# Kernel tuning notes

Hardware: AMD Instinct MI355X
Metric: run time of the kernel (lower is better)

The kernel has to match this reference:

```python
import jax, jax.numpy as jnp
import numpy as np
import math

N = 512  # num particles
D = 128  # particle dimension


def setup_inputs() -> dict:
    key = jax.random.key(0)
    particles = jax.random.normal(key, (N, D), dtype=jnp.float32)
    return {"particles": particles}


def reference(particles):
    # particles: [N, D]
    n = particles.shape[0]
    # delta_x[i, j] = particles[j] - particles[i]  (matches unsqueeze(0) - unsqueeze(1))
    delta_x = particles[None, :, :] - particles[:, None, :]   # [N, N, D]
    norm_sq = delta_x * delta_x                               # [N, N, D]

    # mode='univ': per-dimension median over strictly-upper-triangular pairs
    iu_r, iu_c = np.triu_indices(n, k=1)                      # static indices
    sel = norm_sq[iu_r, iu_c, :]                              # [M, D], M = N(N-1)/2
    m = sel.shape[0]
    # torch.median returns the LOWER of the two middle values for even counts
    median = jnp.sort(sel, axis=0)[(m - 1) // 2]              # [D]

    h = median / math.log(n + 1)
    bandwidth = jnp.maximum(h, jnp.asarray(1e-9, dtype=h.dtype))  # [D]

    log_kernel = -(norm_sq / bandwidth)                       # [N, N, D]
    grad_log_kernel = -2.0 * delta_x / bandwidth              # [N, N, D]
    return log_kernel, grad_log_kernel
```

## Files before the change

kernel.cpp:

```cpp
#include <hip/hip_runtime.h>
#include <hip/hip_bf16.h>

#define NP 512
#define DD 128

__global__ void __launch_bounds__(512)
median_bw_kernel(const float* __restrict__ particles, float* __restrict__ inv_bw)
{
    const int d   = blockIdx.x;
    const int tid = threadIdx.x;

    __shared__ float v[NP];
    __shared__ int   cnt_s[2][8];

    float r = particles[tid * DD + d];

    for (int k = 2; k <= NP; k <<= 1) {
        for (int s = k >> 1; s > 0; s >>= 1) {
            float other;
            if (s < 64) {
                other = __shfl_xor(r, s);
            } else {
                __syncthreads();
                v[tid] = r;
                __syncthreads();
                other = v[tid ^ s];
            }
            const bool lower = (tid & s) == 0;
            const bool up    = (tid & k) == 0;
            r = (lower == up) ? fminf(r, other) : fmaxf(r, other);
        }
    }
    __syncthreads();
    v[tid] = r;
    __syncthreads();

    const float vj = r;
    const int want1 = (NP * (NP - 1) / 2 - 1) / 2 + 1;

    const float maxd = v[NP - 1] - v[0];
    unsigned lo = 0u;
    unsigned hi = __float_as_uint(maxd) + 1u;

    int A = 0, B = tid;
    int buf = 0;

    while (lo < hi) {
        const unsigned mid = (lo + hi) >> 1;
        const float x = __uint_as_float(mid);

        int a = A, b = B;
        while (a < b) {
            const int m = (a + b) >> 1;
            if (vj - v[m] <= x) b = m; else a = m + 1;
        }
        int cnt = tid - a;

        #pragma unroll
        for (int off = 32; off > 0; off >>= 1)
            cnt += __shfl_down(cnt, off);
        if ((tid & 63) == 0) cnt_s[buf][tid >> 6] = cnt;
        __syncthreads();

        int tot = 0;
        #pragma unroll
        for (int w = 0; w < 8; ++w) tot += cnt_s[buf][w];

        if (tot >= want1) { hi = mid;      A = a; }
        else             { lo = mid + 1u; B = a; }
        buf ^= 1;
    }

    if (tid == 0) {
        const float Dk     = __uint_as_float(lo);
        const float median = Dk * Dk;
        const float h      = median / 6.240275844172107f;
        const float bw     = fmaxf(h, 1e-9f);
        inv_bw[d] = 1.0f / bw;
    }
}

__global__ void __launch_bounds__(256)
stein_out_kernel(const float* __restrict__ particles,
                 const float* __restrict__ inv_bw,
                 float4* __restrict__ out_lk,
                 float4* __restrict__ out_g)
{
    const float4* __restrict__ p4  = (const float4*)particles;
    const float4* __restrict__ ib4 = (const float4*)inv_bw;
    const int total = NP * NP * (DD / 4);

    for (int t = blockIdx.x * blockDim.x + threadIdx.x; t < total;
         t += gridDim.x * blockDim.x) {
        const int d4 = t & (DD / 4 - 1);
        const int j  = (t >> 5) & (NP - 1);
        const int i  = t >> 14;

        const float4 xj = p4[j * (DD / 4) + d4];
        const float4 xi = p4[i * (DD / 4) + d4];
        const float4 ib = ib4[d4];

        float4 lk, g;
        {
            const float dx = xj.x - xi.x;
            lk.x = -(dx * dx * ib.x);
            g.x  = -2.0f * dx * ib.x;
        }
        {
            const float dx = xj.y - xi.y;
            lk.y = -(dx * dx * ib.y);
            g.y  = -2.0f * dx * ib.y;
        }
        {
            const float dx = xj.z - xi.z;
            lk.z = -(dx * dx * ib.z);
            g.z  = -2.0f * dx * ib.z;
        }
        {
            const float dx = xj.w - xi.w;
            lk.w = -(dx * dx * ib.w);
            g.w  = -2.0f * dx * ib.w;
        }
        out_lk[t] = lk;
        out_g[t]  = g;
    }
}

extern "C" void kernel_launch(void* const* d_in, const int* in_sizes, int n_in,
                              void* d_out, int out_size, void* d_ws, size_t ws_size,
                              hipStream_t stream)
{
    const float* particles = (const float*)d_in[0];
    float* out    = (float*)d_out;
    float* inv_bw = (float*)d_ws;

    median_bw_kernel<<<DD, 512, 0, stream>>>(particles, inv_bw);

    float4* out_lk = (float4*)out;
    float4* out_g  = (float4*)(out + (size_t)NP * NP * DD);
    stein_out_kernel<<<2048, 256, 0, stream>>>(particles, inv_bw, out_lk, out_g);
}
```

Before: 72.27 us.

## Run median binary search in a single wavefront and use nontemporal output stores

The bandwidth median search now runs on one 64-lane wavefront, with each lane handling eight sorted elements. This removes the per-iteration __syncthreads and the shared-memory count reduction, and uses a wave-wide xor shuffle reduction instead. The output kernel writes both result arrays with nontemporal stores to reduce cache pollution on a large streaming write. The tradeoff is that the median phase now uses less parallelism, since seven of the eight waves sit idle and each lane does eight serial searches per iteration.

```diff
diff --git a/kernel.cpp b/kernel.cpp
--- a/kernel.cpp
+++ b/kernel.cpp
@@ -3,6 +3,8 @@
 
 #define NP 512
 #define DD 128
+
+typedef float f4_ext __attribute__((ext_vector_type(4)));
 
 __global__ void __launch_bounds__(512)
 median_bw_kernel(const float* __restrict__ particles, float* __restrict__ inv_bw)
@@ -11,7 +13,6 @@
     const int tid = threadIdx.x;
 
     __shared__ float v[NP];
-    __shared__ int   cnt_s[2][8];
 
     float r = particles[tid * DD + d];
 
@@ -35,48 +36,72 @@
     v[tid] = r;
     __syncthreads();
 
-    const float vj = r;
-    const int want1 = (NP * (NP - 1) / 2 - 1) / 2 + 1;
+    if (tid < 64) {
+        const int lane  = tid;
+        const int want1 = (NP * (NP - 1) / 2 - 1) / 2 + 1;
 
-    const float maxd = v[NP - 1] - v[0];
-    unsigned lo = 0u;
-    unsigned hi = __float_as_uint(maxd) + 1u;
+        float vj[8];
+        int   A[8], B[8];
+        #pragma unroll
+        for (int w = 0; w < 8; ++w) {
+            const int j = lane + 64 * w;
+            vj[w] = v[j];
+            A[w]  = 0;
+            B[w]  = j;
+        }
 
-    int A = 0, B = tid;
-    int buf = 0;
+        const float maxd = v[NP - 1] - v[0];
+        unsigned lo = 0u;
+        unsigned hi = __float_as_uint(maxd) + 1u;
 
-    while (lo < hi) {
-        const unsigned mid = (lo + hi) >> 1;
-        const float x = __uint_as_float(mid);
+        while (lo < hi) {
+            const unsigned mid = (lo + hi) >> 1;
+            const float x = __uint_as_float(mid);
 
-        int a = A, b = B;
-        while (a < b) {
-            const int m = (a + b) >> 1;
-            if (vj - v[m] <= x) b = m; else a = m + 1;
+            int a[8], b[8];
+            #pragma unroll
+            for (int w = 0; w < 8; ++w) { a[w] = A[w]; b[w] = B[w]; }
+
+            for (int step = 0; step < 10; ++step) {
+                bool any = false;
+                #pragma unroll
+                for (int w = 0; w < 8; ++w) {
+                    if (a[w] < b[w]) {
+                        const int m = (a[w] + b[w]) >> 1;
+                        const float pv = v[m];
+                        if (vj[w] - pv <= x) b[w] = m; else a[w] = m + 1;
+                        any = true;
+                    }
+                }
+                if (!any) break;
+            }
+
+            int cnt = 0;
+            #pragma unroll
+            for (int w = 0; w < 8; ++w) cnt += (lane + 64 * w) - a[w];
+
+            #pragma unroll
+            for (int off = 1; off < 64; off <<= 1)
+                cnt += __shfl_xor(cnt, off);
+
+            if (cnt >= want1) {
+                hi = mid;
+                #pragma unroll
+                for (int w = 0; w < 8; ++w) A[w] = a[w];
+            } else {
+                lo = mid + 1u;
+                #pragma unroll
+                for (int w = 0; w < 8; ++w) B[w] = a[w];
+            }
         }
-        int cnt = tid - a;
 
-        #pragma unroll
-        for (int off = 32; off > 0; off >>= 1)
-            cnt += __shfl_down(cnt, off);
-        if ((tid & 63) == 0) cnt_s[buf][tid >> 6] = cnt;
-        __syncthreads();
-
-        int tot = 0;
-        #pragma unroll
-        for (int w = 0; w < 8; ++w) tot += cnt_s[buf][w];
-
-        if (tot >= want1) { hi = mid;      A = a; }
-        else             { lo = mid + 1u; B = a; }
-        buf ^= 1;
-    }
-
-    if (tid == 0) {
-        const float Dk     = __uint_as_float(lo);
-        const float median = Dk * Dk;
-        const float h      = median / 6.240275844172107f;
-        const float bw     = fmaxf(h, 1e-9f);
-        inv_bw[d] = 1.0f / bw;
+        if (lane == 0) {
+            const float Dk     = __uint_as_float(lo);
+            const float median = Dk * Dk;
+            const float h      = median / 6.240275844172107f;
+            const float bw     = fmaxf(h, 1e-9f);
+            inv_bw[d] = 1.0f / bw;
+        }
     }
 }
 
@@ -121,8 +146,8 @@
             lk.w = -(dx * dx * ib.w);
             g.w  = -2.0f * dx * ib.w;
         }
-        out_lk[t] = lk;
-        out_g[t]  = g;
+        __builtin_nontemporal_store(*(const f4_ext*)&lk, (f4_ext*)&out_lk[t]);
+        __builtin_nontemporal_store(*(const f4_ext*)&g,  (f4_ext*)&out_g[t]);
     }
 }
 
```

Result: slower. 132.0 us (+82.7%).

## Speed median search with order-statistic bracketing, interpolation, and final candidate sort

Applied to the files above, without the earlier changes.

The bisection over float bit patterns for the pairwise-difference median is changed. It now starts from brackets taken from the min and max of fixed-lag sorted differences, alternates interpolation steps with bisection steps, and stops once at most 512 candidate pairs remain. Those candidates are compacted into shared memory with a prefix scan and sorted with a second bitonic sort to select the exact rank. This is meant to cut the number of barrier-synchronized counting rounds in the median kernel. The cost is extra reductions, a scan and a second sort, and the lag-150 bracket heuristic relies on the input distribution for its benefit.

```diff
diff --git a/kernel.cpp b/kernel.cpp
--- a/kernel.cpp
+++ b/kernel.cpp
@@ -4,17 +4,8 @@
 #define NP 512
 #define DD 128
 
-__global__ void __launch_bounds__(512)
-median_bw_kernel(const float* __restrict__ particles, float* __restrict__ inv_bw)
-{
-    const int d   = blockIdx.x;
-    const int tid = threadIdx.x;
-
-    __shared__ float v[NP];
-    __shared__ int   cnt_s[2][8];
-
-    float r = particles[tid * DD + d];
-
+__device__ __forceinline__ float bitonic512(float r, int tid, float* lds)
+{
     for (int k = 2; k <= NP; k <<= 1) {
         for (int s = k >> 1; s > 0; s >>= 1) {
             float other;
@@ -22,15 +13,34 @@
                 other = __shfl_xor(r, s);
             } else {
                 __syncthreads();
-                v[tid] = r;
+                lds[tid] = r;
                 __syncthreads();
-                other = v[tid ^ s];
+                other = lds[tid ^ s];
             }
             const bool lower = (tid & s) == 0;
             const bool up    = (tid & k) == 0;
             r = (lower == up) ? fminf(r, other) : fmaxf(r, other);
         }
     }
+    return r;
+}
+
+__global__ void __launch_bounds__(512)
+median_bw_kernel(const float* __restrict__ particles, float* __restrict__ inv_bw)
+{
+    const int d    = blockIdx.x;
+    const int tid  = threadIdx.x;
+    const int lane = tid & 63;
+    const int wid  = tid >> 6;
+
+    __shared__ float v[NP];
+    __shared__ float cand[NP];
+    __shared__ int   cnt_s[2][8];
+    __shared__ float red_s[2][8];
+    __shared__ int   scan_s[8];
+
+    float r = particles[tid * DD + d];
+    r = bitonic512(r, tid, v);
     __syncthreads();
     v[tid] = r;
     __syncthreads();
@@ -38,45 +48,107 @@
     const float vj = r;
     const int want1 = (NP * (NP - 1) / 2 - 1) / 2 + 1;
 
+    const float d150 = (tid >= 150) ? (vj - v[tid - 150]) : 0.0f;
+    float dmn = (tid >= 150) ? d150 : INFINITY;
+    float dmx = d150;
+    #pragma unroll
+    for (int off = 32; off > 0; off >>= 1) {
+        dmn = fminf(dmn, __shfl_xor(dmn, off));
+        dmx = fmaxf(dmx, __shfl_xor(dmx, off));
+    }
+    if (lane == 0) { red_s[0][wid] = dmn; red_s[1][wid] = dmx; }
+    __syncthreads();
+    float g_mn = INFINITY, g_mx = 0.0f;
+    #pragma unroll
+    for (int w = 0; w < 8; ++w) {
+        g_mn = fminf(g_mn, red_s[0][w]);
+        g_mx = fmaxf(g_mx, red_s[1][w]);
+    }
+
     const float maxd = v[NP - 1] - v[0];
     unsigned lo = 0u;
     unsigned hi = __float_as_uint(maxd) + 1u;
-
+    int C_lo = 0;
+    int C_hi = NP * (NP - 1) / 2;
     int A = 0, B = tid;
-    int buf = 0;
+    int buf = 0, round = 0;
+    int T = C_hi - C_lo;
 
     while (lo < hi) {
-        const unsigned mid = (lo + hi) >> 1;
+        T = C_hi - C_lo;
+        if (T <= NP) break;
+
+        unsigned mid;
+        if (round == 0)      mid = __float_as_uint(g_mn);
+        else if (round == 1) mid = __float_as_uint(g_mx);
+        else if (round & 1) {
+            const float flo  = __uint_as_float(lo);
+            const float fhi  = __uint_as_float(hi);
+            const float frac = (float)(want1 - C_lo) / (float)(C_hi - C_lo);
+            mid = __float_as_uint(flo + (fhi - flo) * frac);
+        } else {
+            mid = lo + ((hi - lo) >> 1);
+        }
+        if (mid < lo)     mid = lo;
+        if (mid > hi - 1) mid = hi - 1;
+
         const float x = __uint_as_float(mid);
-
         int a = A, b = B;
         while (a < b) {
-            const int m = (a + b) >> 1;
-            if (vj - v[m] <= x) b = m; else a = m + 1;
+            const int   m  = (a + b) >> 1;
+            const float pv = v[m];
+            const bool  t  = (vj - pv <= x);
+            b = t ? m : b;
+            a = t ? a : m + 1;
         }
         int cnt = tid - a;
 
         #pragma unroll
-        for (int off = 32; off > 0; off >>= 1)
-            cnt += __shfl_down(cnt, off);
-        if ((tid & 63) == 0) cnt_s[buf][tid >> 6] = cnt;
+        for (int off = 32; off > 0; off >>= 1) cnt += __shfl_down(cnt, off);
+        if (lane == 0) cnt_s[buf][wid] = cnt;
         __syncthreads();
-
         int tot = 0;
         #pragma unroll
         for (int w = 0; w < 8; ++w) tot += cnt_s[buf][w];
 
-        if (tot >= want1) { hi = mid;      A = a; }
-        else             { lo = mid + 1u; B = a; }
+        if (tot >= want1) { hi = mid;      C_hi = tot; A = a; }
+        else              { lo = mid + 1u; C_lo = tot; B = a; }
         buf ^= 1;
-    }
-
-    if (tid == 0) {
-        const float Dk     = __uint_as_float(lo);
-        const float median = Dk * Dk;
-        const float h      = median / 6.240275844172107f;
-        const float bw     = fmaxf(h, 1e-9f);
-        inv_bw[d] = 1.0f / bw;
+        ++round;
+    }
+
+    if (lo >= hi) {
+        if (tid == 0) {
+            const float Dk = __uint_as_float(lo);
+            const float h  = (Dk * Dk) / 6.240275844172107f;
+            inv_bw[d] = 1.0f / fmaxf(h, 1e-9f);
+        }
+    } else {
+        const int rr = want1 - C_lo;
+        const int n  = B - A;
+        int inc = n;
+        #pragma unroll
+        for (int off = 1; off < 64; off <<= 1) {
+            const int t = __shfl_up(inc, off);
+            if (lane >= off) inc += t;
+        }
+        if (lane == 63) scan_s[wid] = inc;
+        __syncthreads();
+        int woff = 0;
+        #pragma unroll
+        for (int w = 0; w < 8; ++w) woff += (w < wid) ? scan_s[w] : 0;
+        int off0 = woff + inc - n;
+        for (int i = A; i < B; ++i) cand[off0++] = vj - v[i];
+        __syncthreads();
+
+        float c = (tid < T) ? cand[tid] : INFINITY;
+        c = bitonic512(c, tid, v);
+
+        if (tid == rr - 1) {
+            const float Dk = c;
+            const float h  = (Dk * Dk) / 6.240275844172107f;
+            inv_bw[d] = 1.0f / fmaxf(h, 1e-9f);
+        }
     }
 }
 
```

New measurement: 71.68 us. About the same (-0.8%).
